# Kernel optimization log

Measured on AMD Instinct MI355X. Metric: run time of the kernel, lower is better.

The kernel has to match this reference:

```python
import jax, jax.numpy as jnp
import numpy as np

NUM_GRAPHS = 64

def setup_inputs() -> dict:
    key = jax.random.key(0)
    ks = jax.random.split(key, 10)
    N, E, D, V = 100000, 1600000, 64, 30
    node_types = jax.random.randint(ks[0], (N,), 0, V, dtype=jnp.int64 if jax.config.jax_enable_x64 else jnp.int32)
    edge_index = jax.random.randint(ks[1], (2, E), 0, N, dtype=jnp.int32)
    batch = jnp.sort(jax.random.randint(ks[2], (N,), 0, NUM_GRAPHS, dtype=jnp.int32))
    emb_table = jax.random.normal(ks[3], (V, D), dtype=jnp.float32)
    W1 = jax.random.normal(ks[4], (D, D), dtype=jnp.float32) / np.sqrt(D)
    W2 = jax.random.normal(ks[5], (D, D), dtype=jnp.float32) / np.sqrt(D)
    W3 = jax.random.normal(ks[6], (D, D), dtype=jnp.float32) / np.sqrt(D)
    b1 = jnp.zeros((D,), jnp.float32)
    b2 = jnp.zeros((D,), jnp.float32)
    b3 = jnp.zeros((D,), jnp.float32)
    return {"node_types": node_types, "edge_index": edge_index, "batch": batch,
            "emb_table": emb_table, "W1": W1, "b1": b1, "W2": W2, "b2": b2, "W3": W3, "b3": b3}

def _gcn_conv(x, W, b, row, col, norm, N):
    # x' = D^-1/2 (A+I) D^-1/2 (x @ W) + b   (PyG GCNConv semantics)
    h = x @ W
    msg = h[row] * norm[:, None]              # gather + edgewise scale
    out = jax.ops.segment_sum(msg, col, num_segments=N)  # scatter-add at targets
    return out + b

def reference(node_types, edge_index, batch, emb_table, W1, b1, W2, b2, W3, b3):
    N = node_types.shape[0]
    # add self-loops
    loops = jnp.arange(N, dtype=edge_index.dtype)
    row = jnp.concatenate([edge_index[0], loops])
    col = jnp.concatenate([edge_index[1], loops])
    # symmetric normalization on A + I
    deg = jax.ops.segment_sum(jnp.ones_like(col, dtype=jnp.float32), col, num_segments=N)
    dinv = jnp.where(deg > 0, jax.lax.rsqrt(deg), 0.0)
    norm = dinv[row] * dinv[col]
    x = emb_table[node_types]
    x = jax.nn.relu(_gcn_conv(x, W1, b1, row, col, norm, N))
    x = jax.nn.relu(_gcn_conv(x, W2, b2, row, col, norm, N))
    x = _gcn_conv(x, W3, b3, row, col, norm, N)
    # global mean pool over batch segments
    sums = jax.ops.segment_sum(x, batch, num_segments=NUM_GRAPHS)
    cnts = jax.ops.segment_sum(jnp.ones((N,), jnp.float32), batch, num_segments=NUM_GRAPHS)
    pooled = sums / jnp.maximum(cnts, 1.0)[:, None]
    # L2 normalize rows
    return pooled / jnp.linalg.norm(pooled, axis=1, keepdims=True)
```

## Files before the change

kernel.cpp:

```cpp
#include <hip/hip_runtime.h>
#include <hip/hip_fp16.h>

#define DD 64
#define NUM_GRAPHS 64
#define AGG_BLOCKS 2048
#define EB 512
#define BINW 256
#define MAXNB 512
#define EBIN_CAP 6144

typedef _Float16 h2_t __attribute__((ext_vector_type(2)));

__device__ __forceinline__ float fdot2u(unsigned a, unsigned b, float c) {
    return __builtin_amdgcn_fdot2(__builtin_bit_cast(h2_t, a),
                                  __builtin_bit_cast(h2_t, b), c, false);
}

__global__ __launch_bounds__(256) void k_hist(const int* __restrict__ col,
                                              int* __restrict__ H, int E, int NB, int CE) {
    __shared__ int h[MAXNB];
    int eb = blockIdx.x, t = threadIdx.x;
    for (int i = t; i < NB; i += 256) h[i] = 0;
    __syncthreads();
    int e0 = eb * CE, e1 = min(E, e0 + CE);
    for (int e = e0 + t; e < e1; e += 256) atomicAdd(&h[col[e] >> 8], 1);
    __syncthreads();
    for (int i = t; i < NB; i += 256) H[eb * NB + i] = h[i];
}

__global__ __launch_bounds__(256) void k_scanA(int* __restrict__ H,
                                               int* __restrict__ bintot, int NB) {
    __shared__ int s[256];
    int b = blockIdx.x, t = threadIdx.x;
    int i0 = (2 * t) * NB + b, i1 = (2 * t + 1) * NB + b;
    int v0 = H[i0], v1 = H[i1];
    int tot = v0 + v1;
    s[t] = tot;
    __syncthreads();
    for (int off = 1; off < 256; off <<= 1) {
        int tv = (t >= off) ? s[t - off] : 0;
        __syncthreads();
        s[t] += tv;
        __syncthreads();
    }
    int excl = s[t] - tot;
    H[i0] = excl;
    H[i1] = excl + v0;
    if (t == 255) bintot[b] = s[255];
}

__global__ void k_scanB(const int* __restrict__ bintot, int* __restrict__ binstart, int NB) {
    __shared__ int s[512];
    int t = threadIdx.x;
    int v = (t < NB) ? bintot[t] : 0;
    s[t] = v;
    __syncthreads();
    for (int off = 1; off < 512; off <<= 1) {
        int tv = (t >= off) ? s[t - off] : 0;
        __syncthreads();
        s[t] += tv;
        __syncthreads();
    }
    if (t < NB) binstart[t] = s[t] - v;
    if (t == 511) binstart[NB] = s[511];
}

__global__ __launch_bounds__(256) void k_scatbin(const int* __restrict__ row,
                                                 const int* __restrict__ col,
                                                 const int* __restrict__ H,
                                                 const int* __restrict__ binstart,
                                                 unsigned* __restrict__ binned,
                                                 int E, int NB, int CE) {
    __shared__ int off[MAXNB];
    int eb = blockIdx.x, t = threadIdx.x;
    for (int i = t; i < NB; i += 256) off[i] = binstart[i] + H[eb * NB + i];
    __syncthreads();
    int e0 = eb * CE, e1 = min(E, e0 + CE);
    for (int e = e0 + t; e < e1; e += 256) {
        int c = col[e], r = row[e];
        int slot = atomicAdd(&off[c >> 8], 1);
        binned[slot] = ((unsigned)(c & 255) << 24) | (unsigned)r;
    }
}

__global__ __launch_bounds__(256) void k_bincsr(const unsigned* __restrict__ binned,
                                                const int* __restrict__ binstart,
                                                const int* __restrict__ nt,
                                                int* __restrict__ srcidx,
                                                int* __restrict__ rowptr,
                                                float* __restrict__ dinv,
                                                int2* __restrict__ pk, int N, int NB) {
    __shared__ unsigned arr[EBIN_CAP];
    __shared__ int sorted_[EBIN_CAP];
    __shared__ int cnt[BINW];
    __shared__ int base[BINW];
    __shared__ int cursor[BINW];
    int b = blockIdx.x, t = threadIdx.x;
    int s0 = binstart[b], s1 = binstart[b + 1];
    int binsz = s1 - s0;
    if (binsz > EBIN_CAP) binsz = EBIN_CAP;
    cnt[t] = 0;
    for (int i = t; i < binsz; i += 256) arr[i] = binned[s0 + i];
    __syncthreads();
    for (int i = t; i < binsz; i += 256) atomicAdd(&cnt[arr[i] >> 24], 1);
    __syncthreads();
    int v = cnt[t];
    base[t] = v;
    __syncthreads();
    for (int off = 1; off < 256; off <<= 1) {
        int tv = (t >= off) ? base[t - off] : 0;
        __syncthreads();
        base[t] += tv;
        __syncthreads();
    }
    int excl = base[t] - v;
    __syncthreads();
    base[t] = excl;
    cursor[t] = excl;
    __syncthreads();
    for (int i = t; i < binsz; i += 256) {
        unsigned val = arr[i];
        int pos = atomicAdd(&cursor[val >> 24], 1);
        sorted_[pos] = (int)(val & 0xFFFFFF);
    }
    __syncthreads();
    for (int i = t; i < binsz; i += 256) srcidx[s0 + i] = sorted_[i];
    int node = b * BINW + t;
    if (node < N) {
        rowptr[node] = s0 + base[t];
        float di = rsqrtf((float)cnt[t] + 1.0f);
        dinv[node] = di;
        pk[node] = make_int2(nt[node], __float_as_int(di));
    }
    if (b == NB - 1 && t == 0) rowptr[N] = s1;
}

__global__ void k_buildepk(const int* __restrict__ srcidx, const int2* __restrict__ pk,
                           unsigned* __restrict__ epku, int E) {
    int i = blockIdx.x * blockDim.x + threadIdx.x;
    if (i >= E) return;
    int2 p = pk[srcidx[i]];
    epku[i] = ((unsigned)p.x << 16) |
              (unsigned)__half_as_ushort(__float2half(__int_as_float(p.y)));
}

__global__ void k_embW1(const float* __restrict__ emb, const float* __restrict__ W1,
                        float* __restrict__ embW1, int V) {
    __shared__ float er[DD];
    int v = blockIdx.x, j = threadIdx.x;
    er[j] = emb[v * DD + j];
    __syncthreads();
    float acc = 0.0f;
    #pragma unroll
    for (int d = 0; d < DD; ++d) acc += er[d] * W1[d * DD + j];
    embW1[v * DD + j] = acc;
}

__global__ void k_packW(const float* __restrict__ W, unsigned* __restrict__ Wpk) {
    int t = blockIdx.x * blockDim.x + threadIdx.x;
    if (t >= 32 * DD) return;
    int p = t >> 6, j = t & 63;
    __half2 h = __floats2half2_rn(W[(2 * p) * DD + j], W[(2 * p + 1) * DD + j]);
    Wpk[t] = __builtin_bit_cast(unsigned, h);
}

__device__ __forceinline__ float epi_dot_q(float4 v, const unsigned* Wc) {
    __half2 h0 = __floats2half2_rn(v.x, v.y);
    __half2 h1 = __floats2half2_rn(v.z, v.w);
    int vp0 = __builtin_bit_cast(int, h0);
    int vp1 = __builtin_bit_cast(int, h1);
    float o0 = 0.f, o1 = 0.f, o2 = 0.f, o3 = 0.f;
    #pragma unroll
    for (int p = 0; p < 32; p += 4) {
        o0 = fdot2u((unsigned)__builtin_amdgcn_readlane(vp0, (p + 0) >> 1), Wc[p + 0], o0);
        o1 = fdot2u((unsigned)__builtin_amdgcn_readlane(vp1, (p + 1) >> 1), Wc[p + 1], o1);
        o2 = fdot2u((unsigned)__builtin_amdgcn_readlane(vp0, (p + 2) >> 1), Wc[p + 2], o2);
        o3 = fdot2u((unsigned)__builtin_amdgcn_readlane(vp1, (p + 3) >> 1), Wc[p + 3], o3);
    }
    return (o0 + o1) + (o2 + o3);
}

__device__ __forceinline__ void acc_h4(float4& a, uint2 r) {
    float2 f0 = __half22float2(*(const __half2*)&r.x);
    float2 f1 = __half22float2(*(const __half2*)&r.y);
    a.x += f0.x; a.y += f0.y; a.z += f1.x; a.w += f1.y;
}

__device__ __forceinline__ float4 gather_sum_q(const int* __restrict__ srcidx,
                                               const __half* __restrict__ Hs,
                                               int s, int e, int g, int l) {
    float4 A = {0,0,0,0}, B = {0,0,0,0}, C = {0,0,0,0}, D = {0,0,0,0};
    int k = s;
    int kend = s + ((e - s) & ~15);
    if (k < kend) {
        uint2 r0 = *(const uint2*)(Hs + (long)srcidx[k + g] * DD + 4 * l);
        uint2 r1 = *(const uint2*)(Hs + (long)srcidx[k + 4 + g] * DD + 4 * l);
        uint2 r2 = *(const uint2*)(Hs + (long)srcidx[k + 8 + g] * DD + 4 * l);
        uint2 r3 = *(const uint2*)(Hs + (long)srcidx[k + 12 + g] * DD + 4 * l);
        k += 16;
        for (; k < kend; k += 16) {
            uint2 n0 = *(const uint2*)(Hs + (long)srcidx[k + g] * DD + 4 * l);
            uint2 n1 = *(const uint2*)(Hs + (long)srcidx[k + 4 + g] * DD + 4 * l);
            uint2 n2 = *(const uint2*)(Hs + (long)srcidx[k + 8 + g] * DD + 4 * l);
            uint2 n3 = *(const uint2*)(Hs + (long)srcidx[k + 12 + g] * DD + 4 * l);
            acc_h4(A, r0); acc_h4(B, r1); acc_h4(C, r2); acc_h4(D, r3);
            r0 = n0; r1 = n1; r2 = n2; r3 = n3;
        }
        acc_h4(A, r0); acc_h4(B, r1); acc_h4(C, r2); acc_h4(D, r3);
    }
    for (; k < e; k += 4) {
        if (k + g < e) {
            uint2 rr = *(const uint2*)(Hs + (long)srcidx[k + g] * DD + 4 * l);
            acc_h4(A, rr);
        }
    }
    A.x += B.x + C.x + D.x; A.y += B.y + C.y + D.y;
    A.z += B.z + C.z + D.z; A.w += B.w + C.w + D.w;
    A.x += __shfl_xor(A.x, 16, 64); A.x += __shfl_xor(A.x, 32, 64);
    A.y += __shfl_xor(A.y, 16, 64); A.y += __shfl_xor(A.y, 32, 64);
    A.z += __shfl_xor(A.z, 16, 64); A.z += __shfl_xor(A.z, 32, 64);
    A.w += __shfl_xor(A.w, 16, 64); A.w += __shfl_xor(A.w, 32, 64);
    return A;
}

__global__ __launch_bounds__(256, 4) void k_agg1_fused(const int* __restrict__ rowptr,
                                                    const unsigned* __restrict__ epku,
                                                    const int2* __restrict__ pk,
                                                    const float* __restrict__ embW1,
                                                    const float* __restrict__ b1,
                                                    __half* __restrict__ OUT, int N, int V) {
    __shared__ float ew[30 * DD];
    int tid = threadIdx.x;
    for (int k = tid; k < V * DD; k += 256) ew[k] = embW1[k];
    __syncthreads();
    int lane = tid & 63;
    int g = lane >> 4, l = lane & 15;
    float4 bq = *(const float4*)(b1 + 4 * l);
    int wave0 = blockIdx.x * 4 + (tid >> 6);
    int wstride = gridDim.x * 4;
    for (int node = __builtin_amdgcn_readfirstlane(wave0); node < N;
         node += wstride) {
        int s = rowptr[node], e = rowptr[node + 1];
        float4 acc = {0.f, 0.f, 0.f, 0.f};
        int k = s;
        for (; k + 8 <= e; k += 8) {
            unsigned u0 = epku[k + g];
            unsigned u1 = epku[k + 4 + g];
            int t0 = u0 >> 16, t1 = u1 >> 16;
            float d0 = __half2float(__ushort_as_half((unsigned short)(u0 & 0xFFFF)));
            float d1 = __half2float(__ushort_as_half((unsigned short)(u1 & 0xFFFF)));
            float4 w0 = *(const float4*)(ew + t0 * DD + 4 * l);
            float4 w1 = *(const float4*)(ew + t1 * DD + 4 * l);
            acc.x += w0.x * d0 + w1.x * d1;
            acc.y += w0.y * d0 + w1.y * d1;
            acc.z += w0.z * d0 + w1.z * d1;
            acc.w += w0.w * d0 + w1.w * d1;
        }
        if (k + 4 <= e) {
            unsigned u0 = epku[k + g];
            int t0 = u0 >> 16;
            float d0 = __half2float(__ushort_as_half((unsigned short)(u0 & 0xFFFF)));
            float4 w0 = *(const float4*)(ew + t0 * DD + 4 * l);
            acc.x += w0.x * d0; acc.y += w0.y * d0;
            acc.z += w0.z * d0; acc.w += w0.w * d0;
            k += 4;
        }
        if (k + g < e) {
            unsigned u0 = epku[k + g];
            int t0 = u0 >> 16;
            float d0 = __half2float(__ushort_as_half((unsigned short)(u0 & 0xFFFF)));
            float4 w0 = *(const float4*)(ew + t0 * DD + 4 * l);
            acc.x += w0.x * d0; acc.y += w0.y * d0;
            acc.z += w0.z * d0; acc.w += w0.w * d0;
        }
        acc.x += __shfl_xor(acc.x, 16, 64); acc.x += __shfl_xor(acc.x, 32, 64);
        acc.y += __shfl_xor(acc.y, 16, 64); acc.y += __shfl_xor(acc.y, 32, 64);
        acc.z += __shfl_xor(acc.z, 16, 64); acc.z += __shfl_xor(acc.z, 32, 64);
        acc.w += __shfl_xor(acc.w, 16, 64); acc.w += __shfl_xor(acc.w, 32, 64);
        int2 pc = pk[node];
        float dc = __int_as_float(pc.y);
        float4 wc = *(const float4*)(ew + pc.x * DD + 4 * l);
        float4 v;
        v.x = fmaxf((acc.x + wc.x * dc) * dc + bq.x, 0.f) * dc;
        v.y = fmaxf((acc.y + wc.y * dc) * dc + bq.y, 0.f) * dc;
        v.z = fmaxf((acc.z + wc.z * dc) * dc + bq.z, 0.f) * dc;
        v.w = fmaxf((acc.w + wc.w * dc) * dc + bq.w, 0.f) * dc;
        if (g == 0) {
            __half2 h0 = __floats2half2_rn(v.x, v.y);
            __half2 h1 = __floats2half2_rn(v.z, v.w);
            uint2 st;
            st.x = __builtin_bit_cast(unsigned, h0);
            st.y = __builtin_bit_cast(unsigned, h1);
            *(uint2*)(OUT + (long)node * DD + 4 * l) = st;
        }
    }
}

__global__ __launch_bounds__(256, 4) void k_agg2_fused(const int* __restrict__ rowptr,
                                                    const int* __restrict__ srcidx,
                                                    const float* __restrict__ dinv,
                                                    const __half* __restrict__ Hs,
                                                    const float* __restrict__ b2,
                                                    const unsigned* __restrict__ W2pk,
                                                    __half* __restrict__ OUT, int N) {
    int tid = threadIdx.x;
    int lane = tid & 63;
    int g = lane >> 4, l = lane & 15;
    unsigned Wc[32];
    #pragma unroll
    for (int p = 0; p < 32; ++p) Wc[p] = W2pk[p * DD + lane];
    float bl = b2[lane];
    int wave0 = blockIdx.x * 4 + (tid >> 6);
    int wstride = gridDim.x * 4;
    for (int node = __builtin_amdgcn_readfirstlane(wave0); node < N;
         node += wstride) {
        int s = rowptr[node], e = rowptr[node + 1];
        float4 acc = gather_sum_q(srcidx, Hs, s, e, g, l);
        float dc = dinv[node];
        uint2 sr = *(const uint2*)(Hs + (long)node * DD + 4 * l);
        float2 s0 = __half22float2(*(const __half2*)&sr.x);
        float2 s1 = __half22float2(*(const __half2*)&sr.y);
        float4 t;
        t.x = (acc.x + s0.x) * dc;
        t.y = (acc.y + s0.y) * dc;
        t.z = (acc.z + s1.x) * dc;
        t.w = (acc.w + s1.y) * dc;
        float u = epi_dot_q(t, Wc);
        float v2 = fmaxf(u + bl, 0.f);
        OUT[(long)node * DD + lane] = __float2half(v2 * dc);
    }
}

__global__ __launch_bounds__(256, 4) void k_agg3_pool(const int* __restrict__ rowptr,
                                                   const int* __restrict__ srcidx,
                                                   const float* __restrict__ dinv,
                                                   const __half* __restrict__ Hs,
                                                   const int* __restrict__ batch,
                                                   float* __restrict__ pool,
                                                   int N, int chunk) {
    int tid = threadIdx.x;
    int lane = tid & 63;
    int g = lane >> 4, l = lane & 15;
    int w = __builtin_amdgcn_readfirstlane(blockIdx.x * 4 + (tid >> 6));
    int start = w * chunk;
    if (start >= N) return;
    int endn = min(N, start + chunk);
    int gcur = batch[start];
    float4 pacc = {0.f, 0.f, 0.f, 0.f};
    for (int node = start; node < endn; ++node) {
        int s = rowptr[node], e = rowptr[node + 1];
        float4 acc = gather_sum_q(srcidx, Hs, s, e, g, l);
        float dc = dinv[node];
        uint2 sr = *(const uint2*)(Hs + (long)node * DD + 4 * l);
        float2 s0 = __half22float2(*(const __half2*)&sr.x);
        float2 s1 = __half22float2(*(const __half2*)&sr.y);
        float4 v;
        v.x = (acc.x + s0.x) * dc;
        v.y = (acc.y + s0.y) * dc;
        v.z = (acc.z + s1.x) * dc;
        v.w = (acc.w + s1.y) * dc;
        int gb = batch[node];
        if (gb != gcur) {
            if (g == 0) {
                atomicAdd(&pool[gcur * DD + 4 * l + 0], pacc.x);
                atomicAdd(&pool[gcur * DD + 4 * l + 1], pacc.y);
                atomicAdd(&pool[gcur * DD + 4 * l + 2], pacc.z);
                atomicAdd(&pool[gcur * DD + 4 * l + 3], pacc.w);
            }
            gcur = gb;
            pacc = v;
        } else {
            pacc.x += v.x; pacc.y += v.y; pacc.z += v.z; pacc.w += v.w;
        }
    }
    if (g == 0) {
        atomicAdd(&pool[gcur * DD + 4 * l + 0], pacc.x);
        atomicAdd(&pool[gcur * DD + 4 * l + 1], pacc.y);
        atomicAdd(&pool[gcur * DD + 4 * l + 2], pacc.z);
        atomicAdd(&pool[gcur * DD + 4 * l + 3], pacc.w);
    }
}

__global__ void k_final(const float* __restrict__ pool, const int* __restrict__ batch,
                        const float* __restrict__ W3, const float* __restrict__ b3,
                        float* __restrict__ out, int N) {
    __shared__ float pr[DD];
    int g = blockIdx.x, j = threadIdx.x;
    pr[j] = pool[g * DD + j];
    __syncthreads();
    int lo = 0, hi = N;
    while (lo < hi) { int m = (lo + hi) >> 1; if (batch[m] < g) lo = m + 1; else hi = m; }
    int lo2 = lo; hi = N;
    while (lo2 < hi) { int m = (lo2 + hi) >> 1; if (batch[m] < g + 1) lo2 = m + 1; else hi = m; }
    float cnt = fmaxf((float)(lo2 - lo), 1.0f);
    float acc = 0.0f;
    #pragma unroll
    for (int d = 0; d < DD; ++d) acc += pr[d] * W3[d * DD + j];
    float v = acc / cnt + b3[j];
    float sq = v * v;
    #pragma unroll
    for (int off = 32; off > 0; off >>= 1) sq += __shfl_down(sq, off, 64);
    float nrm = __shfl(sq, 0, 64);
    out[g * DD + j] = v / sqrtf(nrm);
}

extern "C" void kernel_launch(void* const* d_in, const int* in_sizes, int n_in,
                              void* d_out, int out_size, void* d_ws, size_t ws_size,
                              hipStream_t stream) {
    const int*   node_types = (const int*)d_in[0];
    const int*   edge_index = (const int*)d_in[1];
    const int*   batch      = (const int*)d_in[2];
    const float* emb        = (const float*)d_in[3];
    const float* W1 = (const float*)d_in[4];
    const float* b1 = (const float*)d_in[5];
    const float* W2 = (const float*)d_in[6];
    const float* b2 = (const float*)d_in[7];
    const float* W3 = (const float*)d_in[8];
    const float* b3 = (const float*)d_in[9];
    const int N = in_sizes[0];
    const int E = in_sizes[1] / 2;
    const int V = in_sizes[3] / DD;
    const int* row = edge_index;
    const int* col = edge_index + E;
    const long ND = (long)N * DD;
    const int NB = (N + BINW - 1) / BINW;
    const int CE = (E + EB - 1) / EB;

    char* p = (char*)d_ws;
    __half*   hsA     = (__half*)p;       p += ND * sizeof(__half);
    __half*   hsB     = (__half*)p;       p += ND * sizeof(__half);
    int*      srcidx  = (int*)p;          p += (size_t)E * sizeof(int);
    unsigned* epku    = (unsigned*)p;     p += (size_t)E * sizeof(unsigned);
    unsigned* binned  = (unsigned*)p;     p += (size_t)E * sizeof(unsigned);
    int*      H       = (int*)p;          p += (size_t)EB * NB * sizeof(int);
    int*      bintot  = (int*)p;          p += (size_t)(NB + 4) * sizeof(int);
    int*      binstart= (int*)p;          p += (size_t)(NB + 4) * sizeof(int);
    float*    dinv    = (float*)p;        p += (size_t)N * sizeof(float);
    int2*     pk      = (int2*)p;         p += (size_t)N * sizeof(int2);
    int*      rowptr  = (int*)p;          p += (size_t)(N + 4) * sizeof(int);
    float*    pool    = (float*)p;        p += (size_t)NUM_GRAPHS * DD * sizeof(float);
    float*    embW1   = (float*)p;        p += (size_t)V * DD * sizeof(float);
    unsigned* W2pk    = (unsigned*)p;     p += 32 * DD * sizeof(unsigned);

    k_hist<<<EB, 256, 0, stream>>>(col, H, E, NB, CE);
    k_scanA<<<NB, 256, 0, stream>>>(H, bintot, NB);
    k_scanB<<<1, 512, 0, stream>>>(bintot, binstart, NB);
    k_scatbin<<<EB, 256, 0, stream>>>(row, col, H, binstart, binned, E, NB, CE);
    k_bincsr<<<NB, 256, 0, stream>>>(binned, binstart, node_types, srcidx, rowptr,
                                     dinv, pk, N, NB);
    k_buildepk<<<(E + 255) / 256, 256, 0, stream>>>(srcidx, pk, epku, E);

    k_embW1<<<V, DD, 0, stream>>>(emb, W1, embW1, V);
    k_packW<<<8, 256, 0, stream>>>(W2, W2pk);

    k_agg1_fused<<<AGG_BLOCKS, 256, 0, stream>>>(rowptr, epku, pk, embW1, b1,
                                                 hsA, N, V);
    k_agg2_fused<<<AGG_BLOCKS, 256, 0, stream>>>(rowptr, srcidx, dinv, hsA, b2, W2pk,
                                                 hsB, N);
    hipMemsetAsync(pool, 0, (size_t)(NUM_GRAPHS * DD) * sizeof(float), stream);
    const int totalWaves = AGG_BLOCKS * 4;
    const int chunk = (N + totalWaves - 1) / totalWaves;
    k_agg3_pool<<<AGG_BLOCKS, 256, 0, stream>>>(rowptr, srcidx, dinv, hsB, batch,
                                                pool, N, chunk);
    k_final<<<NUM_GRAPHS, DD, 0, stream>>>(pool, batch, W3, b3, (float*)d_out, N);
}
```

Measured before the change: 293.1 us.

## Widen neighbor gathers to 16-byte loads with 8 edges per wave step

Changes the aggregation layout so each lane loads 8 half values (uint4) per gathered row, with 8 lanes covering a row and 8 edges processed in parallel per wave step. The previous layout used 4-lane groups with 8-byte loads. Layer 2 now prefetches the next node's rowptr range. Layer 3 defers the cross-lane reduction until a pool flush instead of doing it per node. Together these aim to cut memory instructions and shuffle work, at the cost of more register pressure and more tail-handling branches for low-degree nodes.

```diff
diff --git a/kernel.cpp b/kernel.cpp
--- a/kernel.cpp
+++ b/kernel.cpp
@@ -164,63 +164,47 @@
     Wpk[t] = __builtin_bit_cast(unsigned, h);
 }
 
-__device__ __forceinline__ float epi_dot_q(float4 v, const unsigned* Wc) {
-    __half2 h0 = __floats2half2_rn(v.x, v.y);
-    __half2 h1 = __floats2half2_rn(v.z, v.w);
-    int vp0 = __builtin_bit_cast(int, h0);
-    int vp1 = __builtin_bit_cast(int, h1);
-    float o0 = 0.f, o1 = 0.f, o2 = 0.f, o3 = 0.f;
-    #pragma unroll
-    for (int p = 0; p < 32; p += 4) {
-        o0 = fdot2u((unsigned)__builtin_amdgcn_readlane(vp0, (p + 0) >> 1), Wc[p + 0], o0);
-        o1 = fdot2u((unsigned)__builtin_amdgcn_readlane(vp1, (p + 1) >> 1), Wc[p + 1], o1);
-        o2 = fdot2u((unsigned)__builtin_amdgcn_readlane(vp0, (p + 2) >> 1), Wc[p + 2], o2);
-        o3 = fdot2u((unsigned)__builtin_amdgcn_readlane(vp1, (p + 3) >> 1), Wc[p + 3], o3);
-    }
-    return (o0 + o1) + (o2 + o3);
-}
-
-__device__ __forceinline__ void acc_h4(float4& a, uint2 r) {
+__device__ __forceinline__ void acc_h8(float4& A, float4& B, uint4 r) {
     float2 f0 = __half22float2(*(const __half2*)&r.x);
     float2 f1 = __half22float2(*(const __half2*)&r.y);
-    a.x += f0.x; a.y += f0.y; a.z += f1.x; a.w += f1.y;
-}
-
-__device__ __forceinline__ float4 gather_sum_q(const int* __restrict__ srcidx,
-                                               const __half* __restrict__ Hs,
-                                               int s, int e, int g, int l) {
-    float4 A = {0,0,0,0}, B = {0,0,0,0}, C = {0,0,0,0}, D = {0,0,0,0};
+    float2 f2 = __half22float2(*(const __half2*)&r.z);
+    float2 f3 = __half22float2(*(const __half2*)&r.w);
+    A.x += f0.x; A.y += f0.y; A.z += f1.x; A.w += f1.y;
+    B.x += f2.x; B.y += f2.y; B.z += f3.x; B.w += f3.y;
+}
+
+__device__ __forceinline__ void gather_sum_8(const int* __restrict__ srcidx,
+                                             const __half* __restrict__ Hs,
+                                             int s, int e, int g, int l,
+                                             float4& A, float4& B) {
+    float4 A1 = {0.f, 0.f, 0.f, 0.f}, B1 = {0.f, 0.f, 0.f, 0.f};
     int k = s;
     int kend = s + ((e - s) & ~15);
     if (k < kend) {
-        uint2 r0 = *(const uint2*)(Hs + (long)srcidx[k + g] * DD + 4 * l);
-        uint2 r1 = *(const uint2*)(Hs + (long)srcidx[k + 4 + g] * DD + 4 * l);
-        uint2 r2 = *(const uint2*)(Hs + (long)srcidx[k + 8 + g] * DD + 4 * l);
-        uint2 r3 = *(const uint2*)(Hs + (long)srcidx[k + 12 + g] * DD + 4 * l);
+        uint4 r0 = *(const uint4*)(Hs + (long)srcidx[k + g] * DD + 8 * l);
+        uint4 r1 = *(const uint4*)(Hs + (long)srcidx[k + 8 + g] * DD + 8 * l);
         k += 16;
         for (; k < kend; k += 16) {
-            uint2 n0 = *(const uint2*)(Hs + (long)srcidx[k + g] * DD + 4 * l);
-            uint2 n1 = *(const uint2*)(Hs + (long)srcidx[k + 4 + g] * DD + 4 * l);
-            uint2 n2 = *(const uint2*)(Hs + (long)srcidx[k + 8 + g] * DD + 4 * l);
-            uint2 n3 = *(const uint2*)(Hs + (long)srcidx[k + 12 + g] * DD + 4 * l);
-            acc_h4(A, r0); acc_h4(B, r1); acc_h4(C, r2); acc_h4(D, r3);
-            r0 = n0; r1 = n1; r2 = n2; r3 = n3;
-        }
-        acc_h4(A, r0); acc_h4(B, r1); acc_h4(C, r2); acc_h4(D, r3);
-    }
-    for (; k < e; k += 4) {
-        if (k + g < e) {
-            uint2 rr = *(const uint2*)(Hs + (long)srcidx[k + g] * DD + 4 * l);
-            acc_h4(A, rr);
-        }
-    }
-    A.x += B.x + C.x + D.x; A.y += B.y + C.y + D.y;
-    A.z += B.z + C.z + D.z; A.w += B.w + C.w + D.w;
-    A.x += __shfl_xor(A.x, 16, 64); A.x += __shfl_xor(A.x, 32, 64);
-    A.y += __shfl_xor(A.y, 16, 64); A.y += __shfl_xor(A.y, 32, 64);
-    A.z += __shfl_xor(A.z, 16, 64); A.z += __shfl_xor(A.z, 32, 64);
-    A.w += __shfl_xor(A.w, 16, 64); A.w += __shfl_xor(A.w, 32, 64);
-    return A;
+            uint4 n0 = *(const uint4*)(Hs + (long)srcidx[k + g] * DD + 8 * l);
+            uint4 n1 = *(const uint4*)(Hs + (long)srcidx[k + 8 + g] * DD + 8 * l);
+            acc_h8(A, B, r0);
+            acc_h8(A1, B1, r1);
+            r0 = n0; r1 = n1;
+        }
+        acc_h8(A, B, r0);
+        acc_h8(A1, B1, r1);
+    }
+    if (k + 8 <= e) {
+        uint4 r = *(const uint4*)(Hs + (long)srcidx[k + g] * DD + 8 * l);
+        acc_h8(A, B, r);
+        k += 8;
+    }
+    if (k + g < e) {
+        uint4 r = *(const uint4*)(Hs + (long)srcidx[k + g] * DD + 8 * l);
+        acc_h8(A1, B1, r);
+    }
+    A.x += A1.x; A.y += A1.y; A.z += A1.z; A.w += A1.w;
+    B.x += B1.x; B.y += B1.y; B.z += B1.z; B.w += B1.w;
 }
 
 __global__ __launch_bounds__(256, 4) void k_agg1_fused(const int* __restrict__ rowptr,
@@ -305,29 +289,76 @@
                                                     __half* __restrict__ OUT, int N) {
     int tid = threadIdx.x;
     int lane = tid & 63;
-    int g = lane >> 4, l = lane & 15;
+    int g = lane >> 3, l = lane & 7;
     unsigned Wc[32];
     #pragma unroll
     for (int p = 0; p < 32; ++p) Wc[p] = W2pk[p * DD + lane];
     float bl = b2[lane];
-    int wave0 = blockIdx.x * 4 + (tid >> 6);
     int wstride = gridDim.x * 4;
-    for (int node = __builtin_amdgcn_readfirstlane(wave0); node < N;
-         node += wstride) {
-        int s = rowptr[node], e = rowptr[node + 1];
-        float4 acc = gather_sum_q(srcidx, Hs, s, e, g, l);
+    int node = __builtin_amdgcn_readfirstlane(blockIdx.x * 4 + (tid >> 6));
+    int s = 0, e = 0;
+    if (node < N) { s = rowptr[node]; e = rowptr[node + 1]; }
+    while (node < N) {
+        int nn = node + wstride;
+        int ns = 0, ne = 0;
+        if (nn < N) { ns = rowptr[nn]; ne = rowptr[nn + 1]; }
         float dc = dinv[node];
-        uint2 sr = *(const uint2*)(Hs + (long)node * DD + 4 * l);
+        uint4 sr = *(const uint4*)(Hs + (long)node * DD + 8 * l);
+        float4 A = {0.f, 0.f, 0.f, 0.f}, B = {0.f, 0.f, 0.f, 0.f};
+        gather_sum_8(srcidx, Hs, s, e, g, l, A, B);
+        #pragma unroll
+        for (int m = 8; m <= 32; m <<= 1) {
+            A.x += __shfl_xor(A.x, m, 64); A.y += __shfl_xor(A.y, m, 64);
+            A.z += __shfl_xor(A.z, m, 64); A.w += __shfl_xor(A.w, m, 64);
+            B.x += __shfl_xor(B.x, m, 64); B.y += __shfl_xor(B.y, m, 64);
+            B.z += __shfl_xor(B.z, m, 64); B.w += __shfl_xor(B.w, m, 64);
+        }
         float2 s0 = __half22float2(*(const __half2*)&sr.x);
         float2 s1 = __half22float2(*(const __half2*)&sr.y);
-        float4 t;
-        t.x = (acc.x + s0.x) * dc;
-        t.y = (acc.y + s0.y) * dc;
-        t.z = (acc.z + s1.x) * dc;
-        t.w = (acc.w + s1.y) * dc;
-        float u = epi_dot_q(t, Wc);
+        float2 s2 = __half22float2(*(const __half2*)&sr.z);
+        float2 s3 = __half22float2(*(const __half2*)&sr.w);
+        float t0 = (A.x + s0.x) * dc, t1 = (A.y + s0.y) * dc;
+        float t2 = (A.z + s1.x) * dc, t3 = (A.w + s1.y) * dc;
+        float t4 = (B.x + s2.x) * dc, t5 = (B.y + s2.y) * dc;
+        float t6 = (B.z + s3.x) * dc, t7 = (B.w + s3.y) * dc;
+        int vp0 = __builtin_bit_cast(int, __floats2half2_rn(t0, t1));
+        int vp1 = __builtin_bit_cast(int, __floats2half2_rn(t2, t3));
+        int vp2 = __builtin_bit_cast(int, __floats2half2_rn(t4, t5));
+        int vp3 = __builtin_bit_cast(int, __floats2half2_rn(t6, t7));
+        float o0 = 0.f, o1 = 0.f, o2 = 0.f, o3 = 0.f;
+        #pragma unroll
+        for (int p = 0; p < 32; p += 4) {
+            o0 = fdot2u((unsigned)__builtin_amdgcn_readlane(vp0, p >> 2), Wc[p + 0], o0);
+            o1 = fdot2u((unsigned)__builtin_amdgcn_readlane(vp1, p >> 2), Wc[p + 1], o1);
+            o2 = fdot2u((unsigned)__builtin_amdgcn_readlane(vp2, p >> 2), Wc[p + 2], o2);
+            o3 = fdot2u((unsigned)__builtin_amdgcn_readlane(vp3, p >> 2), Wc[p + 3], o3);
+        }
+        float u = (o0 + o1) + (o2 + o3);
         float v2 = fmaxf(u + bl, 0.f);
         OUT[(long)node * DD + lane] = __float2half(v2 * dc);
+        node = nn; s = ns; e = ne;
+    }
+}
+
+__device__ __forceinline__ void flush_pool(float4& PA, float4& PB,
+                                           float* __restrict__ pool,
+                                           int gcur, int g, int l) {
+    #pragma unroll
+    for (int m = 8; m <= 32; m <<= 1) {
+        PA.x += __shfl_xor(PA.x, m, 64); PA.y += __shfl_xor(PA.y, m, 64);
+        PA.z += __shfl_xor(PA.z, m, 64); PA.w += __shfl_xor(PA.w, m, 64);
+        PB.x += __shfl_xor(PB.x, m, 64); PB.y += __shfl_xor(PB.y, m, 64);
+        PB.z += __shfl_xor(PB.z, m, 64); PB.w += __shfl_xor(PB.w, m, 64);
+    }
+    if (g == 0) {
+        atomicAdd(&pool[gcur * DD + 8 * l + 0], PA.x);
+        atomicAdd(&pool[gcur * DD + 8 * l + 1], PA.y);
+        atomicAdd(&pool[gcur * DD + 8 * l + 2], PA.z);
+        atomicAdd(&pool[gcur * DD + 8 * l + 3], PA.w);
+        atomicAdd(&pool[gcur * DD + 8 * l + 4], PB.x);
+        atomicAdd(&pool[gcur * DD + 8 * l + 5], PB.y);
+        atomicAdd(&pool[gcur * DD + 8 * l + 6], PB.z);
+        atomicAdd(&pool[gcur * DD + 8 * l + 7], PB.w);
     }
 }
 
@@ -340,45 +371,41 @@
                                                    int N, int chunk) {
     int tid = threadIdx.x;
     int lane = tid & 63;
-    int g = lane >> 4, l = lane & 15;
+    int g = lane >> 3, l = lane & 7;
     int w = __builtin_amdgcn_readfirstlane(blockIdx.x * 4 + (tid >> 6));
     int start = w * chunk;
     if (start >= N) return;
     int endn = min(N, start + chunk);
     int gcur = batch[start];
-    float4 pacc = {0.f, 0.f, 0.f, 0.f};
+    float4 PA = {0.f, 0.f, 0.f, 0.f}, PB = {0.f, 0.f, 0.f, 0.f};
+    int s = rowptr[start];
     for (int node = start; node < endn; ++node) {
-        int s = rowptr[node], e = rowptr[node + 1];
-        float4 acc = gather_sum_q(srcidx, Hs, s, e, g, l);
+        int e = rowptr[node + 1];
         float dc = dinv[node];
-        uint2 sr = *(const uint2*)(Hs + (long)node * DD + 4 * l);
-        float2 s0 = __half22float2(*(const __half2*)&sr.x);
-        float2 s1 = __half22float2(*(const __half2*)&sr.y);
-        float4 v;
-        v.x = (acc.x + s0.x) * dc;
-        v.y = (acc.y + s0.y) * dc;
-        v.z = (acc.z + s1.x) * dc;
-        v.w = (acc.w + s1.y) * dc;
+        uint4 sr = *(const uint4*)(Hs + (long)node * DD + 8 * l);
         int gb = batch[node];
+        float4 A = {0.f, 0.f, 0.f, 0.f}, B = {0.f, 0.f, 0.f, 0.f};
+        gather_sum_8(srcidx, Hs, s, e, g, l, A, B);
+        if (g == 0) {
+            float2 s0 = __half22float2(*(const __half2*)&sr.x);
+            float2 s1 = __half22float2(*(const __half2*)&sr.y);
+            float2 s2 = __half22float2(*(const __half2*)&sr.z);
+            float2 s3 = __half22float2(*(const __half2*)&sr.w);
+            A.x += s0.x; A.y += s0.y; A.z += s1.x; A.w += s1.y;
+            B.x += s2.x; B.y += s2.y; B.z += s3.x; B.w += s3.y;
+        }
         if (gb != gcur) {
-            if (g == 0) {
-                atomicAdd(&pool[gcur * DD + 4 * l + 0], pacc.x);
-                atomicAdd(&pool[gcur * DD + 4 * l + 1], pacc.y);
-                atomicAdd(&pool[gcur * DD + 4 * l + 2], pacc.z);
-                atomicAdd(&pool[gcur * DD + 4 * l + 3], pacc.w);
-            }
+            flush_pool(PA, PB, pool, gcur, g, l);
             gcur = gb;
-            pacc = v;
+            PA.x = dc * A.x; PA.y = dc * A.y; PA.z = dc * A.z; PA.w = dc * A.w;
+            PB.x = dc * B.x; PB.y = dc * B.y; PB.z = dc * B.z; PB.w = dc * B.w;
         } else {
-            pacc.x += v.x; pacc.y += v.y; pacc.z += v.z; pacc.w += v.w;
-        }
-    }
-    if (g == 0) {
-        atomicAdd(&pool[gcur * DD + 4 * l + 0], pacc.x);
-        atomicAdd(&pool[gcur * DD + 4 * l + 1], pacc.y);
-        atomicAdd(&pool[gcur * DD + 4 * l + 2], pacc.z);
-        atomicAdd(&pool[gcur * DD + 4 * l + 3], pacc.w);
-    }
+            PA.x += dc * A.x; PA.y += dc * A.y; PA.z += dc * A.z; PA.w += dc * A.w;
+            PB.x += dc * B.x; PB.y += dc * B.y; PB.z += dc * B.z; PB.w += dc * B.w;
+        }
+        s = e;
+    }
+    flush_pool(PA, PB, pool, gcur, g, l);
 }
 
 __global__ void k_final(const float* __restrict__ pool, const int* __restrict__ batch,
```

New measurement: 307.8 us. 1.05x slower.
